# Optimization experiments

Measured on AMD Instinct MI355X. Metric: run time of the kernel, lower is better.

## Reference

```python
import jax, jax.numpy as jnp
import numpy as np

B, N, D, H, K = 8, 1024, 1024, 64, 20


def setup_inputs() -> dict:
    key = jax.random.key(0)
    ks = jax.random.split(key, 8)
    s = 0.05
    return {
        "f1": jax.random.normal(ks[0], (B, N, D), jnp.float32),
        "f2": jax.random.normal(ks[1], (B, N, D), jnp.float32),
        "W1a": jax.random.normal(ks[2], (D, H), jnp.float32) * s,
        "b1a": jnp.zeros((H,), jnp.float32),
        "W2a": jax.random.normal(ks[3], (H, H), jnp.float32) * s,
        "b2a": jnp.zeros((H,), jnp.float32),
        "W1b": jax.random.normal(ks[4], (H, H), jnp.float32) * s,
        "b1b": jnp.zeros((H,), jnp.float32),
        "W2b": jax.random.normal(ks[5], (H, H), jnp.float32) * s,
        "b2b": jnp.zeros((H,), jnp.float32),
        "k": K,
    }


def _knn_idx(f, k):
    # f: [N, D] -> indices [N, k] of k nearest neighbors (self excluded)
    sq = jnp.sum(f * f, axis=-1)                      # [N]
    d = sq[:, None] + sq[None, :] - 2.0 * (f @ f.T)   # [N, N] squared dists
    n = f.shape[0]
    d = d + jnp.eye(n, dtype=f.dtype) * jnp.float32(1e10)  # exclude self-loop
    _, idx = jax.lax.top_k(-d, k)                     # smallest distances
    return idx


def _gin_layer(x, idx, W1, b1, W2, b2):
    # GINConv with eps=0: MLP(x + sum_{j in N(i)} x_j)
    agg = jnp.sum(x[idx], axis=1)                     # [N, D] neighbor-sum
    h = x + agg
    h = jnp.maximum(h @ W1 + b1, 0.0) @ W2 + b2
    return h


def reference(f1, f2, W1a, b1a, W2a, b2a, W1b, b1b, W2b, b2b, k):
    def encode(f):
        idx = _knn_idx(f, k)
        h = _gin_layer(f, idx, W1a, b1a, W2a, b2a)
        h = _gin_layer(h, idx, W1b, b1b, W2b, b2b)
        return h

    def per_sample(a, b):
        z1 = encode(a)                                # [N, H]
        z2 = encode(b)                                # [N, H]
        sim = z1 @ z2.T                               # [N, N]
        return jax.nn.softmax(sim, axis=1)

    return jax.vmap(per_sample)(f1, f2)               # [B, N, N]
```

## Files before the change

kernel.cpp:

```cpp
#include <hip/hip_runtime.h>
#include <hip/hip_bf16.h>
#include <math.h>

#define BATCH 8
#define NPTS  1024
#define DIM   1024
#define HID   64
#define KNN   20
#define NMAT  16
#define KPACK 3072

typedef __attribute__((ext_vector_type(8))) short short8;
typedef __attribute__((ext_vector_type(4))) float floatx4;

__device__ __forceinline__ const float* mat_base(const float* f1, const float* f2, int m) {
    return (m < BATCH) ? (f1 + (size_t)m * NPTS * DIM)
                       : (f2 + (size_t)(m - BATCH) * NPTS * DIM);
}

__device__ __forceinline__ unsigned short f2bf_bits(float v) {
    __hip_bfloat16 h = __float2bfloat16(v);
    return *(unsigned short*)&h;
}
__device__ __forceinline__ float bfbits2f(unsigned short b) {
    union { unsigned u; float f; } c; c.u = ((unsigned)b) << 16; return c.f;
}

__global__ __launch_bounds__(256) void split_ymlp_kernel(const float* __restrict__ f1,
                                                         const float* __restrict__ f2,
                                                         const float* __restrict__ W,
                                                         unsigned short* __restrict__ H,
                                                         float* __restrict__ sq,
                                                         float* __restrict__ y) {
    int row0 = blockIdx.x * 64;
    int m = row0 >> 10;
    const float* A = mat_base(f1, f2, m) + (size_t)(row0 & (NPTS - 1)) * DIM;
    unsigned short* Hb = H + (size_t)row0 * KPACK;
    __shared__ float As[64][20];
    __shared__ float Ws[16][HID];
    int tid = threadIdx.x;
    int r = tid >> 2, cq = (tid & 3) * 4;
    int ty = tid >> 4, tx = tid & 15;
    float acc[4][4];
    #pragma unroll
    for (int i = 0; i < 4; ++i)
        #pragma unroll
        for (int j = 0; j < 4; ++j) acc[i][j] = 0.f;
    float sqp = 0.f;
    unsigned short* Hr = Hb + (size_t)r * KPACK + cq;

    for (int kk = 0; kk < DIM; kk += 16) {
        float4 a = *(const float4*)&A[(size_t)r * DIM + kk + cq];
        {
            float vv[4] = {a.x, a.y, a.z, a.w};
            unsigned short h1[4], h2[4], h3[4];
            #pragma unroll
            for (int c = 0; c < 4; ++c) {
                unsigned short b1 = f2bf_bits(vv[c]);
                float r1 = vv[c] - bfbits2f(b1);
                unsigned short b2 = f2bf_bits(r1);
                float r2 = r1 - bfbits2f(b2);
                unsigned short b3 = f2bf_bits(r2);
                h1[c] = b1; h2[c] = b2; h3[c] = b3;
            }
            *(ushort4*)&Hr[kk]        = *(ushort4*)&h1[0];
            *(ushort4*)&Hr[1024 + kk] = *(ushort4*)&h2[0];
            *(ushort4*)&Hr[2048 + kk] = *(ushort4*)&h3[0];
            sqp += a.x * a.x + a.y * a.y + a.z * a.z + a.w * a.w;
        }
        *(float4*)&As[r][cq] = a;
        {
            int d = tid >> 4, hh = (tid & 15) * 4;
            *(float4*)&Ws[d][hh] = *(const float4*)&W[(size_t)(kk + d) * HID + hh];
        }
        __syncthreads();
        #pragma unroll
        for (int k = 0; k < 16; ++k) {
            float av[4];
            #pragma unroll
            for (int ii = 0; ii < 4; ++ii) av[ii] = As[ty * 4 + ii][k];
            float4 w = *(const float4*)&Ws[k][tx * 4];
            #pragma unroll
            for (int ii = 0; ii < 4; ++ii) {
                acc[ii][0] += av[ii] * w.x;
                acc[ii][1] += av[ii] * w.y;
                acc[ii][2] += av[ii] * w.z;
                acc[ii][3] += av[ii] * w.w;
            }
        }
        __syncthreads();
    }
    sqp += __shfl_down(sqp, 1);
    sqp += __shfl_down(sqp, 2);
    if ((tid & 3) == 0) sq[row0 + r] = sqp;
    #pragma unroll
    for (int ii = 0; ii < 4; ++ii)
        *(float4*)&y[(size_t)(row0 + ty * 4 + ii) * HID + tx * 4] = *(float4*)&acc[ii][0];
}

#define GRAM_STEP(CUR, NXT, BUF, T)                                                        \
  {                                                                                        \
    if ((T) < 31) {                                                                        \
      int kn = ((T) + 1) * 32;                                                             \
      _Pragma("unroll")                                                                    \
      for (int s = 0; s < 3; ++s)                                                          \
        _Pragma("unroll")                                                                  \
        for (int a = 0; a < 2; ++a)                                                        \
          NXT[s][a] = *(const short8*)&Hm[(size_t)(ti + ((w << 1) + a) * 16 + r16) * KPACK \
                                          + (size_t)(s << 10) + kn + (kc << 3)];           \
      _Pragma("unroll")                                                                    \
      for (int c = 0; c < 6; ++c) {                                                        \
        int ca = w * 6 + c; int seg = ca >> 3; int rb = ca & 7;                            \
        const unsigned short* gb = Hm + (size_t)(tj + rb * 16 + r16) * KPACK               \
                                      + (size_t)(seg << 10) + kn + (kc << 3);              \
        __builtin_amdgcn_global_load_lds(                                                  \
            (const __attribute__((address_space(1))) void*)gb,                             \
            (__attribute__((address_space(3))) void*)&Bsl[(BUF) ^ 1][ca * 512], 16, 0, 0); \
      }                                                                                    \
      asm volatile("s_waitcnt vmcnt(12)" ::: "memory");                                    \
    } else {                                                                               \
      asm volatile("s_waitcnt vmcnt(0)" ::: "memory");                                     \
    }                                                                                      \
    __builtin_amdgcn_s_barrier();                                                          \
    asm volatile("" ::: "memory");                                                         \
    _Pragma("unroll")                                                                      \
    for (int sb = 0; sb < 3; ++sb) {                                                       \
      short8 bf[8];                                                                        \
      _Pragma("unroll")                                                                    \
      for (int b = 0; b < 8; ++b)                                                          \
        bf[b] = *(const short8*)&Bsl[BUF][(sb * 8 + b) * 512 + lane * 8];                  \
      _Pragma("unroll")                                                                    \
      for (int sa = 0; sa < 3; ++sa) {                                                     \
        if (sa + sb > 2) continue;                                                         \
        _Pragma("unroll")                                                                  \
        for (int a = 0; a < 2; ++a)                                                        \
          _Pragma("unroll")                                                                \
          for (int b = 0; b < 8; ++b)                                                      \
            acc[a][b] = __builtin_amdgcn_mfma_f32_16x16x32_bf16(CUR[sa][a], bf[b],         \
                                                                acc[a][b], 0, 0, 0);       \
      }                                                                                    \
    }                                                                                      \
    asm volatile("" ::: "memory");                                                         \
    __builtin_amdgcn_s_barrier();                                                          \
  }

__global__ __launch_bounds__(256, 2) void gram_mfma_kernel(const unsigned short* __restrict__ H,
                                                           const float* __restrict__ sq,
                                                           float* __restrict__ dist) {
    int bid = blockIdx.x;
    int xcd = bid & 7;
    int g = bid >> 3;
    int m = xcd + 8 * (g & 1);
    int t = g >> 1;
    int bi = 0;
    { int a = t; while (a >= 8 - bi) { a -= 8 - bi; ++bi; } t = a; }
    int bj = bi + t;
    int ti = bi << 7, tj = bj << 7;

    const unsigned short* Hm = H + (size_t)m * NPTS * KPACK;

    __shared__ __align__(16) unsigned short Bsl[2][24 * 512];

    int tid = threadIdx.x;
    int w = tid >> 6, lane = tid & 63;
    int r16 = lane & 15, kc = lane >> 4;

    floatx4 acc[2][8];
    #pragma unroll
    for (int a = 0; a < 2; ++a)
        #pragma unroll
        for (int b = 0; b < 8; ++b) acc[a][b] = (floatx4)0.f;

    short8 afA[3][2], afB[3][2];

    #pragma unroll
    for (int s = 0; s < 3; ++s)
        #pragma unroll
        for (int a = 0; a < 2; ++a)
            afA[s][a] = *(const short8*)&Hm[(size_t)(ti + ((w << 1) + a) * 16 + r16) * KPACK
                                            + (size_t)(s << 10) + (kc << 3)];
    #pragma unroll
    for (int c = 0; c < 6; ++c) {
        int ca = w * 6 + c; int seg = ca >> 3; int rb = ca & 7;
        const unsigned short* gb = Hm + (size_t)(tj + rb * 16 + r16) * KPACK
                                      + (size_t)(seg << 10) + (kc << 3);
        __builtin_amdgcn_global_load_lds(
            (const __attribute__((address_space(1))) void*)gb,
            (__attribute__((address_space(3))) void*)&Bsl[0][ca * 512], 16, 0, 0);
    }

    #pragma unroll 1
    for (int t2 = 0; t2 < 32; t2 += 2) {
        GRAM_STEP(afA, afB, 0, t2);
        GRAM_STEP(afB, afA, 1, t2 + 1);
    }

    const float* sqm = sq + m * NPTS;
    #pragma unroll
    for (int a = 0; a < 2; ++a) {
        int i0 = ti + ((w << 1) + a) * 16 + (lane >> 4) * 4;
        #pragma unroll
        for (int b = 0; b < 8; ++b) {
            int j = tj + b * 16 + (lane & 15);
            float sqj = sqm[j];
            #pragma unroll
            for (int r = 0; r < 4; ++r) {
                int i = i0 + r;
                float v = sqm[i] + sqj - 2.f * acc[a][b][r];
                if (i == j) v += 1e10f;
                dist[((size_t)m * NPTS + i) * NPTS + j] = v;
                if (bi != bj) dist[((size_t)m * NPTS + j) * NPTS + i] = v;
            }
        }
    }
}

__global__ __launch_bounds__(256) void topk_kernel(const float* __restrict__ dist,
                                                   int* __restrict__ knn_idx) {
    int tid = threadIdx.x;
    int wave = tid >> 6, lane = tid & 63;
    int row = blockIdx.x * 4 + wave;
    const float* d = dist + (size_t)row * NPTS;
    float v[16];
    #pragma unroll
    for (int s = 0; s < 16; ++s) v[s] = d[s * 64 + lane];
    int myj = 0;
    for (int sel = 0; sel < KNN; ++sel) {
        float bv = v[0]; int bs = 0;
        #pragma unroll
        for (int s = 1; s < 16; ++s)
            if (v[s] < bv) { bv = v[s]; bs = s; }
        int bj = bs * 64 + lane;
        #pragma unroll
        for (int off = 1; off < 64; off <<= 1) {
            float ov = __shfl_xor(bv, off);
            int   oj = __shfl_xor(bj, off);
            if (ov < bv || (ov == bv && oj < bj)) { bv = ov; bj = oj; }
        }
        if ((bj & 63) == lane) v[bj >> 6] = 3e38f;
        if (lane == sel) myj = bj;
    }
    if (lane < KNN) knn_idx[(size_t)row * KNN + lane] = myj;
}

__global__ __launch_bounds__(256) void t1h1_kernel(const float* __restrict__ y,
                                                   const int* __restrict__ knn_idx,
                                                   const float* __restrict__ W,
                                                   const float* __restrict__ bias1,
                                                   const float* __restrict__ bias2,
                                                   float* __restrict__ h1) {
    int row0 = blockIdx.x * 64;
    int m = row0 >> 10;
    __shared__ int nb[64 * KNN];
    __shared__ float t1s[64][65];
    __shared__ float Ws[64][HID];
    __shared__ float b1s[HID], b2s[HID];
    int tid = threadIdx.x;
    for (int k = tid; k < 64 * KNN; k += 256) nb[k] = knn_idx[(size_t)row0 * KNN + k];
    for (int k = tid; k < 64 * HID; k += 256) Ws[k >> 6][k & 63] = W[k];
    if (tid < HID) { b1s[tid] = bias1[tid]; b2s[tid] = bias2[tid]; }
    __syncthreads();
    {
        int r = tid >> 2, c0 = (tid & 3) * 16;
        const float* yr = y + (size_t)(row0 + r) * HID + c0;
        float4 a[4];
        #pragma unroll
        for (int q = 0; q < 4; ++q) a[q] = *(const float4*)&yr[q * 4];
        const float* ym = y + (size_t)(m << 10) * HID;
        #pragma unroll
        for (int t = 0; t < KNN; ++t) {
            const float* yn = ym + (size_t)nb[r * KNN + t] * HID + c0;
            #pragma unroll
            for (int q = 0; q < 4; ++q) {
                float4 v = *(const float4*)&yn[q * 4];
                a[q].x += v.x; a[q].y += v.y; a[q].z += v.z; a[q].w += v.w;
            }
        }
        #pragma unroll
        for (int q = 0; q < 4; ++q) {
            int c = c0 + q * 4;
            t1s[r][c + 0] = fmaxf(a[q].x + b1s[c + 0], 0.f);
            t1s[r][c + 1] = fmaxf(a[q].y + b1s[c + 1], 0.f);
            t1s[r][c + 2] = fmaxf(a[q].z + b1s[c + 2], 0.f);
            t1s[r][c + 3] = fmaxf(a[q].w + b1s[c + 3], 0.f);
        }
    }
    __syncthreads();
    int ty = tid >> 4, tx = tid & 15;
    float acc[4][4];
    #pragma unroll
    for (int i = 0; i < 4; ++i)
        #pragma unroll
        for (int j = 0; j < 4; ++j) acc[i][j] = 0.f;
    #pragma unroll
    for (int k = 0; k < HID; ++k) {
        float a[4];
        #pragma unroll
        for (int ii = 0; ii < 4; ++ii) a[ii] = t1s[ty * 4 + ii][k];
        float4 w = *(const float4*)&Ws[k][tx * 4];
        #pragma unroll
        for (int ii = 0; ii < 4; ++ii) {
            acc[ii][0] += a[ii] * w.x;
            acc[ii][1] += a[ii] * w.y;
            acc[ii][2] += a[ii] * w.z;
            acc[ii][3] += a[ii] * w.w;
        }
    }
    #pragma unroll
    for (int ii = 0; ii < 4; ++ii) {
        float o[4];
        #pragma unroll
        for (int jj = 0; jj < 4; ++jj) o[jj] = acc[ii][jj] + b2s[tx * 4 + jj];
        *(float4*)&h1[(size_t)(row0 + ty * 4 + ii) * HID + tx * 4] = *(float4*)&o[0];
    }
}

__global__ __launch_bounds__(256) void t2z_kernel(const float* __restrict__ h1,
                                                  const int* __restrict__ knn_idx,
                                                  const float* __restrict__ W1,
                                                  const float* __restrict__ bias1,
                                                  const float* __restrict__ W2,
                                                  const float* __restrict__ bias2,
                                                  float* __restrict__ z) {
    int row0 = blockIdx.x * 64;
    int m = row0 >> 10;
    __shared__ int nb[64 * KNN];
    __shared__ float hs[64][65];
    __shared__ float t2s[64][65];
    __shared__ float Ws[64][HID];
    __shared__ float b1s[HID], b2s[HID];
    int tid = threadIdx.x;
    for (int k = tid; k < 64 * KNN; k += 256) nb[k] = knn_idx[(size_t)row0 * KNN + k];
    for (int k = tid; k < 64 * HID; k += 256) Ws[k >> 6][k & 63] = W1[k];
    if (tid < HID) { b1s[tid] = bias1[tid]; b2s[tid] = bias2[tid]; }
    __syncthreads();
    {
        int r = tid >> 2, c0 = (tid & 3) * 16;
        const float* hr = h1 + (size_t)(row0 + r) * HID + c0;
        float4 a[4];
        #pragma unroll
        for (int q = 0; q < 4; ++q) a[q] = *(const float4*)&hr[q * 4];
        const float* hm = h1 + (size_t)(m << 10) * HID;
        #pragma unroll
        for (int t = 0; t < KNN; ++t) {
            const float* hn = hm + (size_t)nb[r * KNN + t] * HID + c0;
            #pragma unroll
            for (int q = 0; q < 4; ++q) {
                float4 v = *(const float4*)&hn[q * 4];
                a[q].x += v.x; a[q].y += v.y; a[q].z += v.z; a[q].w += v.w;
            }
        }
        #pragma unroll
        for (int q = 0; q < 4; ++q) *(float4*)&hs[r][c0 + q * 4] = a[q];
    }
    __syncthreads();
    int ty = tid >> 4, tx = tid & 15;
    float acc[4][4];
    #pragma unroll
    for (int i = 0; i < 4; ++i)
        #pragma unroll
        for (int j = 0; j < 4; ++j) acc[i][j] = 0.f;
    #pragma unroll
    for (int k = 0; k < HID; ++k) {
        float a[4];
        #pragma unroll
        for (int ii = 0; ii < 4; ++ii) a[ii] = hs[ty * 4 + ii][k];
        float4 w = *(const float4*)&Ws[k][tx * 4];
        #pragma unroll
        for (int ii = 0; ii < 4; ++ii) {
            acc[ii][0] += a[ii] * w.x;
            acc[ii][1] += a[ii] * w.y;
            acc[ii][2] += a[ii] * w.z;
            acc[ii][3] += a[ii] * w.w;
        }
    }
    #pragma unroll
    for (int ii = 0; ii < 4; ++ii)
        #pragma unroll
        for (int jj = 0; jj < 4; ++jj)
            t2s[ty * 4 + ii][tx * 4 + jj] = fmaxf(acc[ii][jj] + b1s[tx * 4 + jj], 0.f);
    __syncthreads();
    for (int k = tid; k < 64 * HID; k += 256) Ws[k >> 6][k & 63] = W2[k];
    __syncthreads();
    #pragma unroll
    for (int i = 0; i < 4; ++i)
        #pragma unroll
        for (int j = 0; j < 4; ++j) acc[i][j] = 0.f;
    #pragma unroll
    for (int k = 0; k < HID; ++k) {
        float a[4];
        #pragma unroll
        for (int ii = 0; ii < 4; ++ii) a[ii] = t2s[ty * 4 + ii][k];
        float4 w = *(const float4*)&Ws[k][tx * 4];
        #pragma unroll
        for (int ii = 0; ii < 4; ++ii) {
            acc[ii][0] += a[ii] * w.x;
            acc[ii][1] += a[ii] * w.y;
            acc[ii][2] += a[ii] * w.z;
            acc[ii][3] += a[ii] * w.w;
        }
    }
    #pragma unroll
    for (int ii = 0; ii < 4; ++ii) {
        float o[4];
        #pragma unroll
        for (int jj = 0; jj < 4; ++jj) o[jj] = acc[ii][jj] + b2s[tx * 4 + jj];
        *(float4*)&z[(size_t)(row0 + ty * 4 + ii) * HID + tx * 4] = *(float4*)&o[0];
    }
}

__global__ __launch_bounds__(256) void sim_kernel(const float* __restrict__ z,
                                                  float* __restrict__ logits) {
    int bid = blockIdx.x;
    int b = bid >> 8;
    int tile = bid & 255;
    int ti = (tile >> 4) << 6;
    int tj = (tile & 15) << 6;
    const float* z1 = z + (size_t)b * NPTS * HID;
    const float* z2 = z + (size_t)(BATCH + b) * NPTS * HID;
    __shared__ float Z1[64][68];
    __shared__ float Z2[64][68];
    int tid = threadIdx.x;
    #pragma unroll
    for (int i = 0; i < 4; ++i) {
        int l = tid + i * 256;
        int r = l >> 4, c = (l & 15) * 4;
        *(float4*)&Z1[r][c] = *(const float4*)&z1[(size_t)(ti + r) * HID + c];
        *(float4*)&Z2[r][c] = *(const float4*)&z2[(size_t)(tj + r) * HID + c];
    }
    __syncthreads();
    int ty = tid >> 4, tx = tid & 15;
    float acc[4][4];
    #pragma unroll
    for (int i = 0; i < 4; ++i)
        #pragma unroll
        for (int j = 0; j < 4; ++j) acc[i][j] = 0.f;
    #pragma unroll
    for (int h = 0; h < HID; ++h) {
        float a[4], bb[4];
        #pragma unroll
        for (int ii = 0; ii < 4; ++ii) { a[ii] = Z1[ty * 4 + ii][h]; bb[ii] = Z2[tx * 4 + ii][h]; }
        #pragma unroll
        for (int ii = 0; ii < 4; ++ii)
            #pragma unroll
            for (int jj = 0; jj < 4; ++jj)
                acc[ii][jj] += a[ii] * bb[jj];
    }
    #pragma unroll
    for (int ii = 0; ii < 4; ++ii) {
        float* dst = logits + ((size_t)b * NPTS + ti + ty * 4 + ii) * NPTS + tj + tx * 4;
        *(float4*)&dst[0] = *(float4*)&acc[ii][0];
    }
}

__global__ __launch_bounds__(256) void softmax_kernel(const float* __restrict__ logits,
                                                      float* __restrict__ out) {
    int row = blockIdx.x;
    const float* L = logits + (size_t)row * NPTS;
    __shared__ float buf[NPTS];
    __shared__ float red[8];
    int tid = threadIdx.x;
    int wave = tid >> 6, lane = tid & 63;
    float mx = -3e38f;
    #pragma unroll
    for (int s = 0; s < 4; ++s) {
        float v = L[tid + s * 256];
        buf[tid + s * 256] = v;
        mx = fmaxf(mx, v);
    }
    #pragma unroll
    for (int off = 32; off > 0; off >>= 1) mx = fmaxf(mx, __shfl_down(mx, off));
    if (lane == 0) red[wave] = mx;
    __syncthreads();
    mx = fmaxf(fmaxf(red[0], red[1]), fmaxf(red[2], red[3]));
    float sum = 0.f;
    #pragma unroll
    for (int s = 0; s < 4; ++s) {
        float e = expf(buf[tid + s * 256] - mx);
        buf[tid + s * 256] = e;
        sum += e;
    }
    #pragma unroll
    for (int off = 32; off > 0; off >>= 1) sum += __shfl_down(sum, off);
    if (lane == 0) red[4 + wave] = sum;
    __syncthreads();
    float inv = 1.f / (red[4] + red[5] + red[6] + red[7]);
    #pragma unroll
    for (int s = 0; s < 4; ++s)
        out[(size_t)row * NPTS + tid + s * 256] = buf[tid + s * 256] * inv;
}

extern "C" void kernel_launch(void* const* d_in, const int* in_sizes, int n_in,
                              void* d_out, int out_size, void* d_ws, size_t ws_size,
                              hipStream_t stream) {
    const float* f1  = (const float*)d_in[0];
    const float* f2  = (const float*)d_in[1];
    const float* W1a = (const float*)d_in[2];
    const float* b1a = (const float*)d_in[3];
    const float* W2a = (const float*)d_in[4];
    const float* b2a = (const float*)d_in[5];
    const float* W1b = (const float*)d_in[6];
    const float* b1b = (const float*)d_in[7];
    const float* W2b = (const float*)d_in[8];
    const float* b2b = (const float*)d_in[9];
    float* out = (float*)d_out;

    char* ws = (char*)d_ws;
    unsigned short* H = (unsigned short*)ws;
    float* dist = (float*)(ws + (size_t)NMAT * NPTS * KPACK * sizeof(unsigned short));
    float* sq   = dist + (size_t)NMAT * NPTS * NPTS;
    int*   kidx = (int*)(sq + NMAT * NPTS);
    float* ybuf = (float*)(kidx + NMAT * NPTS * KNN);
    float* h1b  = ybuf + (size_t)NMAT * NPTS * HID;
    float* zb   = h1b + (size_t)NMAT * NPTS * HID;

    split_ymlp_kernel<<<NMAT * NPTS / 64, 256, 0, stream>>>(f1, f2, W1a, H, sq, ybuf);
    gram_mfma_kernel<<<NMAT * 36, 256, 0, stream>>>(H, sq, dist);
    topk_kernel<<<NMAT * NPTS / 4, 256, 0, stream>>>(dist, kidx);
    t1h1_kernel<<<NMAT * NPTS / 64, 256, 0, stream>>>(ybuf, kidx, W2a, b1a, b2a, h1b);
    t2z_kernel<<<NMAT * NPTS / 64, 256, 0, stream>>>(h1b, kidx, W1b, b1b, W2b, b2b, zb);
    sim_kernel<<<BATCH * 256, 256, 0, stream>>>(zb, dist);
    softmax_kernel<<<BATCH * NPTS, 256, 0, stream>>>(dist, out);
}
```

Baseline: 528.2 us.

## Triple-buffer gram MFMA kernel loads and raise wave priority during MFMA

Deepens the software pipeline in the Gram-matrix MFMA kernel from double to triple buffering. Two k-steps of A fragments and B tiles are now in flight ahead of compute, and the vmcnt waits are adjusted to match. It also raises wave priority with s_setprio around the MFMA block. The aim is to hide global-load latency better, at the cost of 50% more LDS per block and extra registers for a third A fragment set, which may reduce occupancy under the launch bound of 2 blocks per CU.

```diff
diff --git a/kernel.cpp b/kernel.cpp
--- a/kernel.cpp
+++ b/kernel.cpp
@@ -98,37 +98,35 @@
         *(float4*)&y[(size_t)(row0 + ty * 4 + ii) * HID + tx * 4] = *(float4*)&acc[ii][0];
 }
 
-#define GRAM_STEP(CUR, NXT, BUF, T)                                                        \
+#define GRAM_STEP(CURAF, NXTAF, CBUF, NBUF, KN, ISSUE, WAITOP)                             \
   {                                                                                        \
-    if ((T) < 31) {                                                                        \
-      int kn = ((T) + 1) * 32;                                                             \
+    if (ISSUE) {                                                                           \
       _Pragma("unroll")                                                                    \
       for (int s = 0; s < 3; ++s)                                                          \
         _Pragma("unroll")                                                                  \
         for (int a = 0; a < 2; ++a)                                                        \
-          NXT[s][a] = *(const short8*)&Hm[(size_t)(ti + ((w << 1) + a) * 16 + r16) * KPACK \
-                                          + (size_t)(s << 10) + kn + (kc << 3)];           \
+          NXTAF[s][a] = *(const short8*)&Hm[(size_t)(ti + ((w << 1) + a) * 16 + r16) * KPACK \
+                                            + (size_t)(s << 10) + (KN) + (kc << 3)];       \
       _Pragma("unroll")                                                                    \
       for (int c = 0; c < 6; ++c) {                                                        \
         int ca = w * 6 + c; int seg = ca >> 3; int rb = ca & 7;                            \
         const unsigned short* gb = Hm + (size_t)(tj + rb * 16 + r16) * KPACK               \
-                                      + (size_t)(seg << 10) + kn + (kc << 3);              \
+                                      + (size_t)(seg << 10) + (KN) + (kc << 3);            \
         __builtin_amdgcn_global_load_lds(                                                  \
             (const __attribute__((address_space(1))) void*)gb,                             \
-            (__attribute__((address_space(3))) void*)&Bsl[(BUF) ^ 1][ca * 512], 16, 0, 0); \
+            (__attribute__((address_space(3))) void*)&Bsl[NBUF][ca * 512], 16, 0, 0);      \
       }                                                                                    \
-      asm volatile("s_waitcnt vmcnt(12)" ::: "memory");                                    \
-    } else {                                                                               \
-      asm volatile("s_waitcnt vmcnt(0)" ::: "memory");                                     \
     }                                                                                      \
+    asm volatile(WAITOP ::: "memory");                                                     \
     __builtin_amdgcn_s_barrier();                                                          \
     asm volatile("" ::: "memory");                                                         \
+    __builtin_amdgcn_s_setprio(1);                                                         \
     _Pragma("unroll")                                                                      \
     for (int sb = 0; sb < 3; ++sb) {                                                       \
       short8 bf[8];                                                                        \
       _Pragma("unroll")                                                                    \
       for (int b = 0; b < 8; ++b)                                                          \
-        bf[b] = *(const short8*)&Bsl[BUF][(sb * 8 + b) * 512 + lane * 8];                  \
+        bf[b] = *(const short8*)&Bsl[CBUF][(sb * 8 + b) * 512 + lane * 8];                 \
       _Pragma("unroll")                                                                    \
       for (int sa = 0; sa < 3; ++sa) {                                                     \
         if (sa + sb > 2) continue;                                                         \
@@ -136,10 +134,11 @@
         for (int a = 0; a < 2; ++a)                                                        \
           _Pragma("unroll")                                                                \
           for (int b = 0; b < 8; ++b)                                                      \
-            acc[a][b] = __builtin_amdgcn_mfma_f32_16x16x32_bf16(CUR[sa][a], bf[b],         \
+            acc[a][b] = __builtin_amdgcn_mfma_f32_16x16x32_bf16(CURAF[sa][a], bf[b],       \
                                                                 acc[a][b], 0, 0, 0);       \
       }                                                                                    \
     }                                                                                      \
+    __builtin_amdgcn_s_setprio(0);                                                         \
     asm volatile("" ::: "memory");                                                         \
     __builtin_amdgcn_s_barrier();                                                          \
   }
@@ -159,7 +158,7 @@
 
     const unsigned short* Hm = H + (size_t)m * NPTS * KPACK;
 
-    __shared__ __align__(16) unsigned short Bsl[2][24 * 512];
+    __shared__ __align__(16) unsigned short Bsl[3][24 * 512];
 
     int tid = threadIdx.x;
     int w = tid >> 6, lane = tid & 63;
@@ -171,14 +170,16 @@
         #pragma unroll
         for (int b = 0; b < 8; ++b) acc[a][b] = (floatx4)0.f;
 
-    short8 afA[3][2], afB[3][2];
+    short8 afA[3][2], afB[3][2], afC[3][2];
 
     #pragma unroll
     for (int s = 0; s < 3; ++s)
         #pragma unroll
-        for (int a = 0; a < 2; ++a)
-            afA[s][a] = *(const short8*)&Hm[(size_t)(ti + ((w << 1) + a) * 16 + r16) * KPACK
-                                            + (size_t)(s << 10) + (kc << 3)];
+        for (int a = 0; a < 2; ++a) {
+            size_t rowb = (size_t)(ti + ((w << 1) + a) * 16 + r16) * KPACK + (size_t)(s << 10) + (kc << 3);
+            afA[s][a] = *(const short8*)&Hm[rowb];
+            afB[s][a] = *(const short8*)&Hm[rowb + 32];
+        }
     #pragma unroll
     for (int c = 0; c < 6; ++c) {
         int ca = w * 6 + c; int seg = ca >> 3; int rb = ca & 7;
@@ -187,13 +188,19 @@
         __builtin_amdgcn_global_load_lds(
             (const __attribute__((address_space(1))) void*)gb,
             (__attribute__((address_space(3))) void*)&Bsl[0][ca * 512], 16, 0, 0);
+        __builtin_amdgcn_global_load_lds(
+            (const __attribute__((address_space(1))) void*)(gb + 32),
+            (__attribute__((address_space(3))) void*)&Bsl[1][ca * 512], 16, 0, 0);
     }
 
     #pragma unroll 1
-    for (int t2 = 0; t2 < 32; t2 += 2) {
-        GRAM_STEP(afA, afB, 0, t2);
-        GRAM_STEP(afB, afA, 1, t2 + 1);
-    }
+    for (int t2 = 0; t2 < 30; t2 += 3) {
+        GRAM_STEP(afA, afC, 0, 2, (t2 + 2) * 32, 1, "s_waitcnt vmcnt(24)");
+        GRAM_STEP(afB, afA, 1, 0, (t2 + 3) * 32, 1, "s_waitcnt vmcnt(24)");
+        GRAM_STEP(afC, afB, 2, 1, (t2 + 4) * 32, 1, "s_waitcnt vmcnt(24)");
+    }
+    GRAM_STEP(afA, afC, 0, 2, 0, 0, "s_waitcnt vmcnt(12)");
+    GRAM_STEP(afB, afC, 1, 2, 0, 0, "s_waitcnt vmcnt(0)");
 
     const float* sqm = sq + m * NPTS;
     #pragma unroll
```

New measurement: 523.3 us. About the same (-0.9%).
